# Performance work log

Hardware: AMD Instinct MI355X
Metric: run time of the kernel (lower is better)

Reference implementation:

```python
import jax, jax.numpy as jnp
import numpy as np


def _gtconv(A, w):
    # A: [E,N,N], w: [C,E,1,1]; torch: sum(A * softmax(w, dim=1), dim=1) -> [C,N,N]
    s = jax.nn.softmax(w[:, :, 0, 0], axis=1)  # [C,E]
    return jnp.einsum('enm,ce->cnm', A, s)


def _norm_row(H):
    # row-normalize (H + I): D^-1 (H + I)
    n = H.shape[0]
    H = H + jnp.eye(n, dtype=H.dtype)
    deg = jnp.sum(H, axis=1)
    deg = jnp.where(deg <= 1e-10, 1.0, deg)
    return H / deg[:, None]


def _sgc(feature, adj):
    # D^-1/2 (adj + 2I) D^-1/2 @ feature  (diag scaling, same math as torch's dense mm with diag)
    n = adj.shape[0]
    adj = adj + 2.0 * jnp.eye(n, dtype=adj.dtype)
    deg = jnp.sum(adj, axis=1)
    deg = jnp.where(deg <= 1e-10, 1.0, deg)
    dinv = deg ** -0.5
    adj = adj * dinv[:, None] * dinv[None, :]
    return adj @ feature


def setup_inputs() -> dict:
    key = jax.random.key(0)
    ks = jax.random.split(key, 20)
    E, C, N, D, P, F = 5, 2, 3000, 1000, 2000, 128
    inp = {
        'A': jax.random.uniform(ks[0], (E, N, N), dtype=jnp.float32),
        'DTI': jax.random.uniform(ks[1], (N, N), dtype=jnp.float32),
        'drug_structure': jax.random.normal(ks[2], (D, F), dtype=jnp.float32),
        'protein_structure': jax.random.normal(ks[3], (P, F), dtype=jnp.float32),
        'gt_w0a': jax.random.normal(ks[4], (C, E, 1, 1), dtype=jnp.float32),
        'gt_w0b': jax.random.normal(ks[5], (C, E, 1, 1), dtype=jnp.float32),
        'gt_w1': jax.random.normal(ks[6], (C, E, 1, 1), dtype=jnp.float32),
        'a_param': jnp.ones((C + 1, 1, 1), dtype=jnp.float32),
        'drug_num': D,
        'protein_num': P,
    }
    lin_keys = jax.random.split(ks[7], 12)
    names = ['wd1', 'bd1', 'wd2', 'bd2', 'wd3', 'bd3', 'wp1', 'bp1', 'wp2', 'bp2', 'wp3', 'bp3']
    for i, nm in enumerate(names):
        shp = (F, F) if nm.startswith('w') else (F,)
        inp[nm] = jax.random.normal(lin_keys[i], shp, dtype=jnp.float32) * 0.05
    return inp


def reference(A, DTI, drug_structure, protein_structure, gt_w0a, gt_w0b, gt_w1,
              wd1, bd1, wd2, bd2, wd3, bd3, wp1, bp1, wp2, bp2, wp3, bp3,
              a_param, drug_num, protein_num):
    relu = jax.nn.relu
    drug = relu(drug_structure @ wd1.T + bd1)
    drug = relu(drug @ wd2.T + bd2)
    drug = relu(drug @ wd3.T + bd3)
    prot = relu(protein_structure @ wp1.T + bp1)
    prot = relu(prot @ wp2.T + bp2)
    prot = relu(prot @ wp3.T + bp3)
    feature = jnp.concatenate([drug, prot], axis=0)  # [N,128]

    # GT layers: layer 0 (first=True), layer 1 (first=False)
    a0 = _gtconv(A, gt_w0a)  # [C,N,N]
    b0 = _gtconv(A, gt_w0b)
    H = jnp.matmul(a0, b0)  # bmm
    H = jax.vmap(_norm_row)(H)
    H = jnp.matmul(H, _gtconv(A, gt_w1))

    adj = H  # H[:, :N, :N] is a no-op here
    X_conv1 = _sgc(_sgc(feature, DTI), DTI)
    chs = jax.vmap(lambda a_: _sgc(_sgc(feature, a_), a_))(adj)  # [C,N,128]

    C = adj.shape[0]
    if C == 1:
        X_conv3 = chs
    else:
        order = [0, 1]
        for i in range(2, C):
            order = [i] + order  # torch prepends X_tem for i>=2
        X_conv3 = chs[jnp.array(order)]

    X_conv = jnp.concatenate([X_conv1[None], X_conv3], axis=0)  # [C+1,N,128]
    att = jax.nn.softmax(a_param, axis=0)  # [C+1,1,1]
    conv_sum = jnp.sum(att * X_conv, axis=0)  # [N,128]

    drug_feature = conv_sum[:drug_num]
    protein_feature = conv_sum[drug_num:]
    y = jax.nn.sigmoid(drug_feature @ protein_feature.T)  # [D,P]
    return y
```

## Files before the change

### kernel.cpp

```cpp
#include <hip/hip_runtime.h>
#include <hip/hip_bf16.h>

typedef __attribute__((ext_vector_type(8))) __bf16 bf16x8;
typedef __attribute__((ext_vector_type(4))) float floatx4;

#define NVALID 3000
#define NPAD   3072
#define FEA    128
#define ZSPLIT 8
#define KCHUNK 384
#define PSTRIDE 393216
#define SLOT   ((size_t)ZSPLIT * PSTRIDE)

__device__ __forceinline__ void gload16(const void* g, void* l) {
    __builtin_amdgcn_global_load_lds(
        (const __attribute__((address_space(1))) void*)g,
        (__attribute__((address_space(3))) void*)l,
        16, 0, 0);
}

__device__ __forceinline__ float b2f(__hip_bfloat16 h) { return __bfloat162float(h); }

__global__ __launch_bounds__(256) void mlp_fused(
    const float* __restrict__ Xd, const float* __restrict__ Xp,
    const float* __restrict__ Wd1, const float* __restrict__ bd1,
    const float* __restrict__ Wd2, const float* __restrict__ bd2,
    const float* __restrict__ Wd3, const float* __restrict__ bd3,
    const float* __restrict__ Wp1, const float* __restrict__ bp1,
    const float* __restrict__ Wp2, const float* __restrict__ bp2,
    const float* __restrict__ Wp3, const float* __restrict__ bp3,
    float* __restrict__ Y)
{
    const bool isP = blockIdx.x >= 125;
    const float* X  = isP ? Xp : Xd;
    const float* W1 = isP ? Wp1 : Wd1; const float* b1 = isP ? bp1 : bd1;
    const float* W2 = isP ? Wp2 : Wd2; const float* b2 = isP ? bp2 : bd2;
    const float* W3 = isP ? Wp3 : Wd3; const float* b3 = isP ? bp3 : bd3;
    const int m0loc = (isP ? (blockIdx.x - 125) : blockIdx.x) * 8;
    const int m0out = blockIdx.x * 8;

    __shared__ float S0[8][128], S1[8][128];
    const int t = threadIdx.x;
    for (int s2 = t; s2 < 1024; s2 += 256) {
        int r = s2 >> 7, ii = s2 & 127;
        S0[r][ii] = X[(size_t)(m0loc + r) * 128 + ii];
    }
    __syncthreads();
    const int o = t & 127, rh = t >> 7;

    {
        float a0 = 0.f, a1 = 0.f, a2 = 0.f, a3 = 0.f;
        const float* wr = W1 + (size_t)o * 128;
        for (int i = 0; i < 128; ++i) {
            float w = wr[i];
            a0 += S0[rh + 0][i] * w; a1 += S0[rh + 2][i] * w;
            a2 += S0[rh + 4][i] * w; a3 += S0[rh + 6][i] * w;
        }
        float bo = b1[o];
        S1[rh + 0][o] = fmaxf(a0 + bo, 0.f);
        S1[rh + 2][o] = fmaxf(a1 + bo, 0.f);
        S1[rh + 4][o] = fmaxf(a2 + bo, 0.f);
        S1[rh + 6][o] = fmaxf(a3 + bo, 0.f);
    }
    __syncthreads();
    {
        float a0 = 0.f, a1 = 0.f, a2 = 0.f, a3 = 0.f;
        const float* wr = W2 + (size_t)o * 128;
        for (int i = 0; i < 128; ++i) {
            float w = wr[i];
            a0 += S1[rh + 0][i] * w; a1 += S1[rh + 2][i] * w;
            a2 += S1[rh + 4][i] * w; a3 += S1[rh + 6][i] * w;
        }
        float bo = b2[o];
        S0[rh + 0][o] = fmaxf(a0 + bo, 0.f);
        S0[rh + 2][o] = fmaxf(a1 + bo, 0.f);
        S0[rh + 4][o] = fmaxf(a2 + bo, 0.f);
        S0[rh + 6][o] = fmaxf(a3 + bo, 0.f);
    }
    __syncthreads();
    {
        float a0 = 0.f, a1 = 0.f, a2 = 0.f, a3 = 0.f;
        const float* wr = W3 + (size_t)o * 128;
        for (int i = 0; i < 128; ++i) {
            float w = wr[i];
            a0 += S0[rh + 0][i] * w; a1 += S0[rh + 2][i] * w;
            a2 += S0[rh + 4][i] * w; a3 += S0[rh + 6][i] * w;
        }
        float bo = b3[o];
        Y[(size_t)(m0out + rh + 0) * 128 + o] = fmaxf(a0 + bo, 0.f);
        Y[(size_t)(m0out + rh + 2) * 128 + o] = fmaxf(a1 + bo, 0.f);
        Y[(size_t)(m0out + rh + 4) * 128 + o] = fmaxf(a2 + bo, 0.f);
        Y[(size_t)(m0out + rh + 6) * 128 + o] = fmaxf(a3 + bo, 0.f);
    }
}

__device__ __forceinline__ void softmax5(const float* __restrict__ w, float* s)
{
    float m = w[0];
    #pragma unroll
    for (int e = 1; e < 5; ++e) m = fmaxf(m, w[e]);
    float sum = 0.f;
    #pragma unroll
    for (int e = 0; e < 5; ++e) { s[e] = __expf(w[e] - m); sum += s[e]; }
    float r = 1.f / sum;
    #pragma unroll
    for (int e = 0; e < 5; ++e) s[e] *= r;
}

__global__ __launch_bounds__(384) void gtconv_fused(
    const float* __restrict__ A, const float* __restrict__ w0a,
    const float* __restrict__ w0b, const float* __restrict__ w1,
    __hip_bfloat16* __restrict__ a00, __hip_bfloat16* __restrict__ b00,
    __hip_bfloat16* __restrict__ g10,
    __hip_bfloat16* __restrict__ a01, __hip_bfloat16* __restrict__ b01,
    __hip_bfloat16* __restrict__ g11,
    float* __restrict__ r1v)
{
    float sw[6][5];
    softmax5(w0a + 0, sw[0]); softmax5(w0b + 0, sw[1]); softmax5(w1 + 0, sw[2]);
    softmax5(w0a + 5, sw[3]); softmax5(w0b + 5, sw[4]); softmax5(w1 + 5, sw[5]);

    const int i  = blockIdx.x;
    const int t  = threadIdx.x;
    const int j0 = t * 8;
    float acc[6][8] = {};
    if (i < NVALID && j0 < NVALID) {
        #pragma unroll
        for (int e = 0; e < 5; ++e) {
            const float* Ae = A + (size_t)e * 9000000 + (size_t)i * 3000 + j0;
            float4 v0 = *reinterpret_cast<const float4*>(Ae);
            float4 v1 = *reinterpret_cast<const float4*>(Ae + 4);
            float x[8] = { v0.x, v0.y, v0.z, v0.w, v1.x, v1.y, v1.z, v1.w };
            #pragma unroll
            for (int m = 0; m < 6; ++m) {
                float se = sw[m][e];
                #pragma unroll
                for (int u = 0; u < 8; ++u) acc[m][u] += se * x[u];
            }
        }
    }
    __hip_bfloat16* dsts[6] = { a00, b00, g10, a01, b01, g11 };
    const size_t base = (size_t)i * NPAD + j0;
    float rs[4];
    #pragma unroll
    for (int m = 0; m < 6; ++m) {
        __align__(16) __hip_bfloat16 h[8];
        float s = 0.f;
        #pragma unroll
        for (int u = 0; u < 8; ++u) {
            h[u] = __float2bfloat16(acc[m][u]);
            s += b2f(h[u]);
        }
        *reinterpret_cast<uint4*>(&dsts[m][base]) = *reinterpret_cast<const uint4*>(h);
        if (m == 1) rs[0] = s; else if (m == 2) rs[1] = s;
        else if (m == 4) rs[2] = s; else if (m == 5) rs[3] = s;
    }
    __shared__ float red[6][4];
    #pragma unroll
    for (int q = 0; q < 4; ++q) {
        float s = rs[q];
        #pragma unroll
        for (int off = 32; off > 0; off >>= 1) s += __shfl_down(s, off);
        if ((t & 63) == 0) red[t >> 6][q] = s;
    }
    __syncthreads();
    if (t == 0) {
        #pragma unroll
        for (int q = 0; q < 4; ++q) {
            float s = red[0][q] + red[1][q] + red[2][q]
                    + red[3][q] + red[4][q] + red[5][q];
            r1v[(size_t)q * NPAD + i] = s;
        }
    }
}

__global__ __launch_bounds__(256) void matvec_degA(
    const __hip_bfloat16* __restrict__ a0_0, const __hip_bfloat16* __restrict__ a0_1,
    const __hip_bfloat16* __restrict__ b0_0, const __hip_bfloat16* __restrict__ b0_1,
    const float* __restrict__ r1v,
    float* __restrict__ dinv2, float* __restrict__ mv12)
{
    const int y = blockIdx.y;
    const __hip_bfloat16* M = (y == 0) ? a0_0 : (y == 1) ? a0_1 : (y == 2) ? b0_0 : b0_1;
    const float* v = (y == 0) ? r1v : (y == 1) ? r1v + 2 * NPAD
                   : (y == 2) ? r1v + NPAD : r1v + 3 * NPAD;
    const size_t i = blockIdx.x;
    const int t = threadIdx.x;
    const __hip_bfloat16* row = M + i * NPAD;
    float s = 0.f;
    for (int k = t * 8; k < NPAD; k += 2048) {
        uint4 u = *reinterpret_cast<const uint4*>(&row[k]);
        const unsigned short* us = reinterpret_cast<const unsigned short*>(&u);
        #pragma unroll
        for (int e = 0; e < 8; ++e)
            s += __uint_as_float(((unsigned int)us[e]) << 16) * v[k + e];
    }
    #pragma unroll
    for (int off = 32; off > 0; off >>= 1) s += __shfl_down(s, off);
    __shared__ float red[4];
    if ((t & 63) == 0) red[t >> 6] = s;
    __syncthreads();
    if (t == 0) {
        float tot = red[0] + red[1] + red[2] + red[3];
        if (y < 2) dinv2[(size_t)y * NPAD + i] = 1.f / (tot + 1.f);
        else       mv12[(size_t)(y - 2) * NPAD + i] = tot;
    }
}

__global__ __launch_bounds__(256) void matvec_degB(
    const __hip_bfloat16* __restrict__ a0_0, const __hip_bfloat16* __restrict__ a0_1,
    const float* __restrict__ mv12, const float* __restrict__ dinv2,
    const float* __restrict__ r1v, float* __restrict__ rsv2)
{
    const int c = blockIdx.y;
    const __hip_bfloat16* M = c ? a0_1 : a0_0;
    const float* v = mv12 + (size_t)c * NPAD;
    const float* add = r1v + (size_t)(2 * c + 1) * NPAD;
    const size_t i = blockIdx.x;
    const int t = threadIdx.x;
    const __hip_bfloat16* row = M + i * NPAD;
    float s = 0.f;
    for (int k = t * 8; k < NPAD; k += 2048) {
        uint4 u = *reinterpret_cast<const uint4*>(&row[k]);
        const unsigned short* us = reinterpret_cast<const unsigned short*>(&u);
        #pragma unroll
        for (int e = 0; e < 8; ++e)
            s += __uint_as_float(((unsigned int)us[e]) << 16) * v[k + e];
    }
    #pragma unroll
    for (int off = 32; off > 0; off >>= 1) s += __shfl_down(s, off);
    __shared__ float red[4];
    if ((t & 63) == 0) red[t >> 6] = s;
    __syncthreads();
    if (t == 0) {
        float tot = red[0] + red[1] + red[2] + red[3];
        rsv2[(size_t)c * NPAD + i] =
            rsqrtf(dinv2[(size_t)c * NPAD + i] * (tot + add[i]) + 2.f);
    }
}

__global__ __launch_bounds__(256) void rowdeg_f32(
    const float* __restrict__ src, float* __restrict__ outv)
{
    const int i = blockIdx.x, t = threadIdx.x;
    float s = 0.f;
    if (i < NVALID) {
        const float* row = src + (size_t)i * 3000;
        for (int j4 = t; j4 < 750; j4 += 256) {
            float4 v = *reinterpret_cast<const float4*>(row + j4 * 4);
            s += v.x + v.y + v.z + v.w;
        }
    }
    #pragma unroll
    for (int off = 32; off > 0; off >>= 1) s += __shfl_down(s, off);
    __shared__ float red[4];
    if ((t & 63) == 0) red[t >> 6] = s;
    __syncthreads();
    if (t == 0) {
        float tot = red[0] + red[1] + red[2] + red[3];
        outv[i] = rsqrtf(tot + 2.f);
    }
}

__global__ __launch_bounds__(256) void scale_cast_f32(
    const float* __restrict__ src, int lds_, int nvalid,
    const float* __restrict__ vec, __hip_bfloat16* __restrict__ dst)
{
    const int i = blockIdx.y;
    const int j0 = (blockIdx.x * 256 + threadIdx.x) * 4;
    const float vi = vec[i];
    float v[4];
    if (i < nvalid && j0 + 3 < nvalid) {
        float4 f = *reinterpret_cast<const float4*>(src + (size_t)i * lds_ + j0);
        v[0] = f.x; v[1] = f.y; v[2] = f.z; v[3] = f.w;
    } else {
        #pragma unroll
        for (int u = 0; u < 4; ++u) {
            int j = j0 + u;
            v[u] = (i < nvalid && j < nvalid) ? src[(size_t)i * lds_ + j] : 0.f;
        }
    }
    #pragma unroll
    for (int u = 0; u < 4; ++u) {
        int j = j0 + u;
        if (j == i && i < nvalid) v[u] += 2.f;
        v[u] *= vi * vec[j];
    }
    __align__(8) __hip_bfloat16 h[4];
    #pragma unroll
    for (int u = 0; u < 4; ++u) h[u] = __float2bfloat16(v[u]);
    *reinterpret_cast<uint2*>(&dst[(size_t)i * NPAD + j0]) =
        *reinterpret_cast<const uint2*>(h);
}

__global__ __launch_bounds__(256) void transpose_feat(
    const float* __restrict__ X, int nvalid, __hip_bfloat16* __restrict__ XT)
{
    __shared__ float Ts[32][33];
    const int k0 = blockIdx.x * 32, n0 = blockIdx.y * 32;
    const int t = threadIdx.x, tr = t >> 5, tc = t & 31;
    #pragma unroll
    for (int p = 0; p < 4; ++p) {
        int k = k0 + tr + p * 8;
        Ts[tr + p * 8][tc] = (k < nvalid) ? X[(size_t)k * 128 + n0 + tc] : 0.f;
    }
    __syncthreads();
    #pragma unroll
    for (int p = 0; p < 4; ++p) {
        int n = tr + p * 8;
        XT[(size_t)(n0 + n) * NPAD + k0 + tc] = __float2bfloat16(Ts[tc][n]);
    }
}

__global__ __launch_bounds__(256) void scale_colsT2(
    const __hip_bfloat16* __restrict__ XT, const float* __restrict__ rsv2,
    __hip_bfloat16* __restrict__ W0T_0, __hip_bfloat16* __restrict__ W0T_1)
{
    const int c = blockIdx.z;
    const float* s = rsv2 + (size_t)c * NPAD;
    __hip_bfloat16* W0T = c ? W0T_1 : W0T_0;
    const int f = blockIdx.y;
    const int k0 = (blockIdx.x * 256 + threadIdx.x) * 8;
    if (k0 >= NPAD) return;
    uint4 u = *reinterpret_cast<const uint4*>(&XT[(size_t)f * NPAD + k0]);
    const unsigned short* us = reinterpret_cast<const unsigned short*>(&u);
    __align__(16) __hip_bfloat16 h[8];
    #pragma unroll
    for (int e = 0; e < 8; ++e) {
        float x = __uint_as_float(((unsigned int)us[e]) << 16);
        h[e] = __float2bfloat16(x * s[k0 + e]);
    }
    *reinterpret_cast<uint4*>(&W0T[(size_t)f * NPAD + k0]) =
        *reinterpret_cast<const uint4*>(h);
}

__global__ __launch_bounds__(256, 3) void gemm_pan_batch(
    const __hip_bfloat16* __restrict__ P0, const __hip_bfloat16* __restrict__ M0,
    const __hip_bfloat16* __restrict__ P1, const __hip_bfloat16* __restrict__ M1,
    const __hip_bfloat16* __restrict__ P2, const __hip_bfloat16* __restrict__ M2,
    __hip_bfloat16* __restrict__ part)
{
    const int b  = blockIdx.z / ZSPLIT;
    const int zz = blockIdx.z % ZSPLIT;
    const __hip_bfloat16* P = (b == 0) ? P0 : (b == 1) ? P1 : P2;
    const __hip_bfloat16* M = (b == 0) ? M0 : (b == 1) ? M1 : M2;
    __hip_bfloat16* C = part + (size_t)b * SLOT + (size_t)zz * PSTRIDE;

    __shared__ __align__(16) __hip_bfloat16 As[128 * 32];
    __shared__ __align__(16) __hip_bfloat16 Bs[128 * 32];
    const int t = threadIdx.x;
    const int lane = t & 63;
    const int w = t >> 6;
    const int wm = w >> 1, wn = w & 1;
    const int tn = blockIdx.x;
    const int kbeg = zz * KCHUNK;

    const int srow = lane >> 2;
    const int skg  = (lane & 3) * 8;
    const __hip_bfloat16* Ag = P + (size_t)(w * 32 + srow) * NPAD + skg;
    const __hip_bfloat16* Bg = M + (size_t)(tn * 128 + w * 32 + srow) * NPAD + skg;
    __hip_bfloat16* Al0 = &As[w * 1024];
    __hip_bfloat16* Al1 = &As[w * 1024 + 512];
    __hip_bfloat16* Bl0 = &Bs[w * 1024];
    __hip_bfloat16* Bl1 = &Bs[w * 1024 + 512];

    floatx4 acc[4][4] = {};
// ... 78 lines not shown
        for (int ni = 0; ni < 4; ++ni)
            bfv[ni] = *reinterpret_cast<const bf16x8*>(
                &Bs[(wn * 64 + ni * 16 + (lane & 15)) * 32 + koff]);
        #pragma unroll
        for (int mi = 0; mi < 4; ++mi)
            #pragma unroll
            for (int ni = 0; ni < 4; ++ni)
                acc[mi][ni] = __builtin_amdgcn_mfma_f32_16x16x32_bf16(
                    af[mi], bfv[ni], acc[mi][ni], 0, 0, 0);
    }

    const int r0 = tm * 128 + wm * 64 + ((lane >> 4) << 2);
    const int c0 = tn * 128 + wn * 64 + (lane & 15);
    #pragma unroll
    for (int mi = 0; mi < 4; ++mi)
        #pragma unroll
        for (int ni = 0; ni < 4; ++ni) {
            const int col = c0 + ni * 16;
            #pragma unroll
            for (int r = 0; r < 4; ++r) {
                const int row = r0 + mi * 16 + r;
                if (row < Mvalid && col < Nvalid)
                    C[(size_t)row * ldc + col] =
                        1.f / (1.f + __expf(-acc[mi][ni][r]));
            }
        }
}

__global__ __launch_bounds__(256) void reduce_sum_b(
    const __hip_bfloat16* __restrict__ part,
    __hip_bfloat16* __restrict__ O0, __hip_bfloat16* __restrict__ O1,
    __hip_bfloat16* __restrict__ O2)
{
    const int b = blockIdx.y;
    __hip_bfloat16* O = (b == 0) ? O0 : (b == 1) ? O1 : O2;
    if (!O) return;
    const __hip_bfloat16* Pp = part + (size_t)b * SLOT;
    const size_t idx = ((size_t)blockIdx.x * 256 + threadIdx.x) * 8;
    float s[8] = {};
    #pragma unroll
    for (int z = 0; z < ZSPLIT; ++z) {
        uint4 u = *reinterpret_cast<const uint4*>(&Pp[(size_t)z * PSTRIDE + idx]);
        const unsigned short* us = reinterpret_cast<const unsigned short*>(&u);
        #pragma unroll
        for (int e = 0; e < 8; ++e)
            s[e] += __uint_as_float(((unsigned int)us[e]) << 16);
    }
    __align__(16) __hip_bfloat16 h[8];
    #pragma unroll
    for (int e = 0; e < 8; ++e) h[e] = __float2bfloat16(s[e]);
    *reinterpret_cast<uint4*>(&O[idx]) = *reinterpret_cast<const uint4*>(h);
}

__global__ __launch_bounds__(256) void reduce_att_T(
    const __hip_bfloat16* __restrict__ part, const float* __restrict__ ap,
    float* __restrict__ conv)
{
    __shared__ float Ts[32][33];
    const int i0 = blockIdx.x * 32, f0 = blockIdx.y * 32;
    const int t = threadIdx.x, tr = t >> 5, tc = t & 31;
    float a0 = ap[0], a1 = ap[1], a2 = ap[2];
    float m = fmaxf(a0, fmaxf(a1, a2));
    float e0 = __expf(a0 - m), e1 = __expf(a1 - m), e2 = __expf(a2 - m);
    float att0 = e0 / (e0 + e1 + e2);
    #pragma unroll
    for (int p = 0; p < 4; ++p) {
        int f = f0 + tr + p * 8;
        float s = 0.f;
        #pragma unroll
        for (int z = 0; z < ZSPLIT; ++z)
            s += b2f(part[(size_t)z * PSTRIDE + (size_t)f * NPAD + i0 + tc]);
        Ts[tr + p * 8][tc] = s;
    }
    __syncthreads();
    #pragma unroll
    for (int p = 0; p < 4; ++p) {
        int i = i0 + tr + p * 8;
        conv[(size_t)i * 128 + f0 + tc] = att0 * Ts[tc][tr + p * 8];
    }
}

__global__ __launch_bounds__(256) void combine_mid2(
    const __hip_bfloat16* __restrict__ part,
    const __hip_bfloat16* __restrict__ Z0, const __hip_bfloat16* __restrict__ Z1,
    const __hip_bfloat16* __restrict__ XTF,
    const float* __restrict__ rsv2, const float* __restrict__ dinv2,
    __hip_bfloat16* __restrict__ Wp0, __hip_bfloat16* __restrict__ Wp1)
{
    const int c = blockIdx.y;
    const __hip_bfloat16* Vp = part + (size_t)c * SLOT;
    const __hip_bfloat16* Z  = c ? Z1 : Z0;
    const float* sv = rsv2 + (size_t)c * NPAD;
    const float* dv = dinv2 + (size_t)c * NPAD;
    __hip_bfloat16* Wp = c ? Wp1 : Wp0;

    const size_t idx = ((size_t)blockIdx.x * 256 + threadIdx.x) * 8;
    const int i = (int)(idx % NPAD);
    float s[8] = {};
    #pragma unroll
    for (int z = 0; z < ZSPLIT; ++z) {
        uint4 u = *reinterpret_cast<const uint4*>(&Vp[(size_t)z * PSTRIDE + idx]);
        const unsigned short* us = reinterpret_cast<const unsigned short*>(&u);
        #pragma unroll
        for (int e = 0; e < 8; ++e)
            s[e] += __uint_as_float(((unsigned int)us[e]) << 16);
    }
    uint4 uz = *reinterpret_cast<const uint4*>(&Z[idx]);
    uint4 ux = *reinterpret_cast<const uint4*>(&XTF[idx]);
    const unsigned short* usz = reinterpret_cast<const unsigned short*>(&uz);
    const unsigned short* usx = reinterpret_cast<const unsigned short*>(&ux);
    __align__(16) __hip_bfloat16 h[8];
    #pragma unroll
    for (int e = 0; e < 8; ++e) {
        float vsum = s[e] + __uint_as_float(((unsigned int)usz[e]) << 16);
        float x    = __uint_as_float(((unsigned int)usx[e]) << 16);
        float si = sv[i + e], di = dv[i + e];
        float out1 = si * di * vsum + 2.f * si * si * x;
        h[e] = __float2bfloat16(si * out1);
    }
    *reinterpret_cast<uint4*>(&Wp[idx]) = *reinterpret_cast<const uint4*>(h);
}

__global__ __launch_bounds__(256) void combine_att2_T(
    const __hip_bfloat16* __restrict__ part,
    const __hip_bfloat16* __restrict__ Z2_0, const __hip_bfloat16* __restrict__ Z2_1,
    const __hip_bfloat16* __restrict__ Wp0, const __hip_bfloat16* __restrict__ Wp1,
    const float* __restrict__ rsv2, const float* __restrict__ dinv2,
    const float* __restrict__ ap, float* __restrict__ conv)
{
    __shared__ float Ts[32][33];
    const int i0 = blockIdx.x * 32, f0 = blockIdx.y * 32;
    const int t = threadIdx.x, tr = t >> 5, tc = t & 31;
    float a0 = ap[0], a1 = ap[1], a2 = ap[2];
    float m = fmaxf(a0, fmaxf(a1, a2));
    float e0 = __expf(a0 - m), e1 = __expf(a1 - m), e2 = __expf(a2 - m);
    float inv = 1.f / (e0 + e1 + e2);
    float att1 = e1 * inv, att2 = e2 * inv;
    const int i = i0 + tc;
    float s0i = rsv2[i],        d0i = dinv2[i];
    float s1i = rsv2[NPAD + i], d1i = dinv2[NPAD + i];
    #pragma unroll
    for (int p = 0; p < 4; ++p) {
        int f = f0 + tr + p * 8;
        size_t fi = (size_t)f * NPAD + i;
        float v0 = b2f(Z2_0[fi]);
        float v1 = b2f(Z2_1[fi]);
        #pragma unroll
        for (int z = 0; z < ZSPLIT; ++z) {
            v0 += b2f(part[(size_t)z * PSTRIDE + fi]);
            v1 += b2f(part[SLOT + (size_t)z * PSTRIDE + fi]);
        }
        float o0 = s0i * d0i * v0 + 2.f * s0i * b2f(Wp0[fi]);
        float o1 = s1i * d1i * v1 + 2.f * s1i * b2f(Wp1[fi]);
        Ts[tr + p * 8][tc] = att1 * o0 + att2 * o1;
    }
    __syncthreads();
    #pragma unroll
    for (int p = 0; p < 4; ++p) {
        int i2 = i0 + tr + p * 8;
        conv[(size_t)i2 * 128 + f0 + tc] += Ts[tc][tr + p * 8];
    }
}

__global__ __launch_bounds__(256) void cast_split(
    const float* __restrict__ acc, __hip_bfloat16* __restrict__ dF,
    __hip_bfloat16* __restrict__ pF)
{
    const int idx = blockIdx.x * 256 + threadIdx.x;
    if (idx < 1024 * 128) {
        int r = idx >> 7;
        dF[idx] = __float2bfloat16(r < 1000 ? acc[idx] : 0.f);
    } else {
        int j = idx - 1024 * 128;
        int r = j >> 7;
        pF[j] = __float2bfloat16(r < 2000 ? acc[(size_t)(1000 + r) * 128 + (j & 127)] : 0.f);
    }
}

extern "C" void kernel_launch(void* const* d_in, const int* in_sizes, int n_in,
                              void* d_out, int out_size, void* d_ws, size_t ws_size,
                              hipStream_t stream)
{
    const float* A     = (const float*)d_in[0];
    const float* DTI   = (const float*)d_in[1];
    const float* drugS = (const float*)d_in[2];
    const float* protS = (const float*)d_in[3];
    const float* w0a   = (const float*)d_in[4];
    const float* w0b   = (const float*)d_in[5];
    const float* w1g   = (const float*)d_in[6];
    const float* ap    = (const float*)d_in[7];
    const float* wd1 = (const float*)d_in[10]; const float* bd1 = (const float*)d_in[11];
    const float* wd2 = (const float*)d_in[12]; const float* bd2 = (const float*)d_in[13];
    const float* wd3 = (const float*)d_in[14]; const float* bd3 = (const float*)d_in[15];
    const float* wp1 = (const float*)d_in[16]; const float* bp1 = (const float*)d_in[17];
    const float* wp2 = (const float*)d_in[18]; const float* bp2 = (const float*)d_in[19];
    const float* wp3 = (const float*)d_in[20]; const float* bp3 = (const float*)d_in[21];
    float* out = (float*)d_out;

    const size_t SQ_BF  = (size_t)NPAD * NPAD * 2;
    const size_t PAN_BF = (size_t)128 * NPAD * 2;
    char* p = (char*)d_ws;
    auto alloc = [&](size_t sz) { char* r = p; p += (sz + 255) & ~(size_t)255; return r; };
    __hip_bfloat16* sdti = (__hip_bfloat16*)alloc(SQ_BF);
    __hip_bfloat16* a0c[2], *b0c[2], *g1c[2];
    for (int c = 0; c < 2; ++c) {
        a0c[c] = (__hip_bfloat16*)alloc(SQ_BF);
        b0c[c] = (__hip_bfloat16*)alloc(SQ_BF);
        g1c[c] = (__hip_bfloat16*)alloc(SQ_BF);
    }
    __hip_bfloat16* part = (__hip_bfloat16*)alloc((size_t)3 * SLOT * 2);
    float* r1v   = (float*)alloc((size_t)4 * NPAD * 4);
    float* dinv2 = (float*)alloc((size_t)2 * NPAD * 4);
    float* mv12  = (float*)alloc((size_t)2 * NPAD * 4);
    float* rsv2  = (float*)alloc((size_t)2 * NPAD * 4);
    float* degv  = (float*)alloc((size_t)NPAD * 4);
    float* fb    = (float*)alloc((size_t)NPAD * 128 * 4);
    float* conv  = (float*)alloc((size_t)NPAD * 128 * 4);
    __hip_bfloat16* XTF  = (__hip_bfloat16*)alloc(PAN_BF);
    __hip_bfloat16* XT2  = (__hip_bfloat16*)alloc(PAN_BF);
    __hip_bfloat16* W0T_0 = (__hip_bfloat16*)alloc(PAN_BF);
    __hip_bfloat16* W0T_1 = (__hip_bfloat16*)alloc(PAN_BF);
    __hip_bfloat16* Z_0  = (__hip_bfloat16*)alloc(PAN_BF);
    __hip_bfloat16* Z_1  = (__hip_bfloat16*)alloc(PAN_BF);
    __hip_bfloat16* U_0  = (__hip_bfloat16*)alloc(PAN_BF);
    __hip_bfloat16* U_1  = (__hip_bfloat16*)alloc(PAN_BF);
    __hip_bfloat16* Wp_0 = (__hip_bfloat16*)alloc(PAN_BF);
    __hip_bfloat16* Wp_1 = (__hip_bfloat16*)alloc(PAN_BF);
    __hip_bfloat16* dF = (__hip_bfloat16*)alloc((size_t)1024 * 128 * 2);
    __hip_bfloat16* pF = (__hip_bfloat16*)alloc((size_t)2048 * 128 * 2);
    if ((size_t)(p - (char*)d_ws) > ws_size) return;

    mlp_fused<<<375, 256, 0, stream>>>(drugS, protS,
        wd1, bd1, wd2, bd2, wd3, bd3, wp1, bp1, wp2, bp2, wp3, bp3, fb);
    transpose_feat<<<dim3(96, 4), 256, 0, stream>>>(fb, 3000, XTF);

    gtconv_fused<<<NPAD, 384, 0, stream>>>(A, w0a, w0b, w1g,
        a0c[0], b0c[0], g1c[0], a0c[1], b0c[1], g1c[1], r1v);

    rowdeg_f32<<<NPAD, 256, 0, stream>>>(DTI, degv);
    scale_cast_f32<<<dim3(3, NPAD), 256, 0, stream>>>(DTI, 3000, 3000, degv, sdti);

    matvec_degA<<<dim3(NPAD, 4), 256, 0, stream>>>(a0c[0], a0c[1], b0c[0], b0c[1],
        r1v, dinv2, mv12);
    matvec_degB<<<dim3(NPAD, 2), 256, 0, stream>>>(a0c[0], a0c[1], mv12, dinv2, r1v, rsv2);
    scale_colsT2<<<dim3(2, 128, 2), 256, 0, stream>>>(XTF, rsv2, W0T_0, W0T_1);

    gemm_pan_batch<<<dim3(24, 1, 3 * ZSPLIT), 256, 0, stream>>>(
        XTF, sdti, W0T_0, g1c[0], W0T_1, g1c[1], part);
    reduce_sum_b<<<dim3(192, 3), 256, 0, stream>>>(part, XT2, Z_0, Z_1);

    gemm_pan_batch<<<dim3(24, 1, 3 * ZSPLIT), 256, 0, stream>>>(
        XT2, sdti, Z_0, b0c[0], Z_1, b0c[1], part);
    reduce_att_T<<<dim3(96, 4), 256, 0, stream>>>(part, ap, conv);
    reduce_sum_b<<<dim3(192, 2), 256, 0, stream>>>(part + SLOT, U_0, U_1, nullptr);

    gemm_pan_batch<<<dim3(24, 1, 2 * ZSPLIT), 256, 0, stream>>>(
        U_0, a0c[0], U_1, a0c[1], nullptr, nullptr, part);
    combine_mid2<<<dim3(192, 2), 256, 0, stream>>>(part, Z_0, Z_1, XTF,
        rsv2, dinv2, Wp_0, Wp_1);

    gemm_pan_batch<<<dim3(24, 1, 2 * ZSPLIT), 256, 0, stream>>>(
        Wp_0, g1c[0], Wp_1, g1c[1], nullptr, nullptr, part);
    reduce_sum_b<<<dim3(192, 2), 256, 0, stream>>>(part, Z_0, Z_1, nullptr);
    gemm_pan_batch<<<dim3(24, 1, 2 * ZSPLIT), 256, 0, stream>>>(
        Z_0, b0c[0], Z_1, b0c[1], nullptr, nullptr, part);
    reduce_sum_b<<<dim3(192, 2), 256, 0, stream>>>(part, U_0, U_1, nullptr);
    gemm_pan_batch<<<dim3(24, 1, 2 * ZSPLIT), 256, 0, stream>>>(
        U_0, a0c[0], U_1, a0c[1], nullptr, nullptr, part);
    combine_att2_T<<<dim3(96, 4), 256, 0, stream>>>(part, Z_0, Z_1, Wp_0, Wp_1,
        rsv2, dinv2, ap, conv);

    cast_split<<<1536, 256, 0, stream>>>(conv, dF, pF);
    gemm_sig<<<dim3(16, 8), 256, 0, stream>>>(dF, pF, out, 128, 128, 128, 2000, 1000, 2000);
}
```

Baseline: 267.4 us.

## Merge independent small kernels into horizontally fused launches to cut launch count

Independent kernels are merged into combined launches that branch on block index. The gtconv, DTI row-degree and MLP work become one kernel, and the feature transpose, DTI scale-cast and degree matvec become another. The two reductions after the second GEMM are merged, and the final attention combine now writes the bf16 split outputs directly, removing cast_split. The aim is to cut kernel launch and tail overhead and one round trip of conv through memory, at the cost of heterogeneous blocks sharing one launch configuration, with the MLP branch leaving 128 of its 384 threads idle.

```diff
diff --git a/kernel.cpp b/kernel.cpp
--- a/kernel.cpp
+++ b/kernel.cpp
@@ -21,7 +21,28 @@
 
 __device__ __forceinline__ float b2f(__hip_bfloat16 h) { return __bfloat162float(h); }
 
-__global__ __launch_bounds__(256) void mlp_fused(
+__device__ __forceinline__ void softmax5(const float* __restrict__ w, float* s)
+{
+    float m = w[0];
+    #pragma unroll
+    for (int e = 1; e < 5; ++e) m = fmaxf(m, w[e]);
+    float sum = 0.f;
+    #pragma unroll
+    for (int e = 0; e < 5; ++e) { s[e] = __expf(w[e] - m); sum += s[e]; }
+    float r = 1.f / sum;
+    #pragma unroll
+    for (int e = 0; e < 5; ++e) s[e] *= r;
+}
+
+__global__ __launch_bounds__(384) void head_fused(
+    const float* __restrict__ A, const float* __restrict__ w0a,
+    const float* __restrict__ w0b, const float* __restrict__ w1,
+    __hip_bfloat16* __restrict__ a00, __hip_bfloat16* __restrict__ b00,
+    __hip_bfloat16* __restrict__ g10,
+    __hip_bfloat16* __restrict__ a01, __hip_bfloat16* __restrict__ b01,
+    __hip_bfloat16* __restrict__ g11,
+    float* __restrict__ r1v,
+    const float* __restrict__ DTI, float* __restrict__ degv,
     const float* __restrict__ Xd, const float* __restrict__ Xp,
     const float* __restrict__ Wd1, const float* __restrict__ bd1,
     const float* __restrict__ Wd2, const float* __restrict__ bd2,
@@ -31,179 +52,229 @@
     const float* __restrict__ Wp3, const float* __restrict__ bp3,
     float* __restrict__ Y)
 {
-    const bool isP = blockIdx.x >= 125;
-    const float* X  = isP ? Xp : Xd;
-    const float* W1 = isP ? Wp1 : Wd1; const float* b1 = isP ? bp1 : bd1;
-    const float* W2 = isP ? Wp2 : Wd2; const float* b2 = isP ? bp2 : bd2;
-    const float* W3 = isP ? Wp3 : Wd3; const float* b3 = isP ? bp3 : bd3;
-    const int m0loc = (isP ? (blockIdx.x - 125) : blockIdx.x) * 8;
-    const int m0out = blockIdx.x * 8;
-
-    __shared__ float S0[8][128], S1[8][128];
+    const int bid = blockIdx.x;
     const int t = threadIdx.x;
-    for (int s2 = t; s2 < 1024; s2 += 256) {
-        int r = s2 >> 7, ii = s2 & 127;
-        S0[r][ii] = X[(size_t)(m0loc + r) * 128 + ii];
-    }
-    __syncthreads();
-    const int o = t & 127, rh = t >> 7;
-
-    {
-        float a0 = 0.f, a1 = 0.f, a2 = 0.f, a3 = 0.f;
-        const float* wr = W1 + (size_t)o * 128;
-        for (int i = 0; i < 128; ++i) {
-            float w = wr[i];
-            a0 += S0[rh + 0][i] * w; a1 += S0[rh + 2][i] * w;
-            a2 += S0[rh + 4][i] * w; a3 += S0[rh + 6][i] * w;
-        }
-        float bo = b1[o];
-        S1[rh + 0][o] = fmaxf(a0 + bo, 0.f);
-        S1[rh + 2][o] = fmaxf(a1 + bo, 0.f);
-        S1[rh + 4][o] = fmaxf(a2 + bo, 0.f);
-        S1[rh + 6][o] = fmaxf(a3 + bo, 0.f);
-    }
-    __syncthreads();
-    {
-        float a0 = 0.f, a1 = 0.f, a2 = 0.f, a3 = 0.f;
-        const float* wr = W2 + (size_t)o * 128;
-        for (int i = 0; i < 128; ++i) {
-            float w = wr[i];
-            a0 += S1[rh + 0][i] * w; a1 += S1[rh + 2][i] * w;
-            a2 += S1[rh + 4][i] * w; a3 += S1[rh + 6][i] * w;
-        }
-        float bo = b2[o];
-        S0[rh + 0][o] = fmaxf(a0 + bo, 0.f);
-        S0[rh + 2][o] = fmaxf(a1 + bo, 0.f);
-        S0[rh + 4][o] = fmaxf(a2 + bo, 0.f);
-        S0[rh + 6][o] = fmaxf(a3 + bo, 0.f);
-    }
-    __syncthreads();
-    {
-        float a0 = 0.f, a1 = 0.f, a2 = 0.f, a3 = 0.f;
-        const float* wr = W3 + (size_t)o * 128;
-        for (int i = 0; i < 128; ++i) {
-            float w = wr[i];
-            a0 += S0[rh + 0][i] * w; a1 += S0[rh + 2][i] * w;
-            a2 += S0[rh + 4][i] * w; a3 += S0[rh + 6][i] * w;
-        }
-        float bo = b3[o];
-        Y[(size_t)(m0out + rh + 0) * 128 + o] = fmaxf(a0 + bo, 0.f);
-        Y[(size_t)(m0out + rh + 2) * 128 + o] = fmaxf(a1 + bo, 0.f);
-        Y[(size_t)(m0out + rh + 4) * 128 + o] = fmaxf(a2 + bo, 0.f);
-        Y[(size_t)(m0out + rh + 6) * 128 + o] = fmaxf(a3 + bo, 0.f);
-    }
-}
-
-__device__ __forceinline__ void softmax5(const float* __restrict__ w, float* s)
-{
-    float m = w[0];
-    #pragma unroll
-    for (int e = 1; e < 5; ++e) m = fmaxf(m, w[e]);
-    float sum = 0.f;
-    #pragma unroll
-    for (int e = 0; e < 5; ++e) { s[e] = __expf(w[e] - m); sum += s[e]; }
-    float r = 1.f / sum;
-    #pragma unroll
-    for (int e = 0; e < 5; ++e) s[e] *= r;
-}
-
-__global__ __launch_bounds__(384) void gtconv_fused(
-    const float* __restrict__ A, const float* __restrict__ w0a,
-    const float* __restrict__ w0b, const float* __restrict__ w1,
-    __hip_bfloat16* __restrict__ a00, __hip_bfloat16* __restrict__ b00,
-    __hip_bfloat16* __restrict__ g10,
-    __hip_bfloat16* __restrict__ a01, __hip_bfloat16* __restrict__ b01,
-    __hip_bfloat16* __restrict__ g11,
-    float* __restrict__ r1v)
-{
-    float sw[6][5];
-    softmax5(w0a + 0, sw[0]); softmax5(w0b + 0, sw[1]); softmax5(w1 + 0, sw[2]);
-    softmax5(w0a + 5, sw[3]); softmax5(w0b + 5, sw[4]); softmax5(w1 + 5, sw[5]);
-
-    const int i  = blockIdx.x;
-    const int t  = threadIdx.x;
-    const int j0 = t * 8;
-    float acc[6][8] = {};
-    if (i < NVALID && j0 < NVALID) {
-        #pragma unroll
-        for (int e = 0; e < 5; ++e) {
-            const float* Ae = A + (size_t)e * 9000000 + (size_t)i * 3000 + j0;
-            float4 v0 = *reinterpret_cast<const float4*>(Ae);
-            float4 v1 = *reinterpret_cast<const float4*>(Ae + 4);
-            float x[8] = { v0.x, v0.y, v0.z, v0.w, v1.x, v1.y, v1.z, v1.w };
-            #pragma unroll
-            for (int m = 0; m < 6; ++m) {
-                float se = sw[m][e];
+
+    if (bid < NPAD) {
+        float sw[6][5];
+        softmax5(w0a + 0, sw[0]); softmax5(w0b + 0, sw[1]); softmax5(w1 + 0, sw[2]);
+        softmax5(w0a + 5, sw[3]); softmax5(w0b + 5, sw[4]); softmax5(w1 + 5, sw[5]);
+
+        const int i  = bid;
+        const int j0 = t * 8;
+        float acc[6][8] = {};
+        if (i < NVALID && j0 < NVALID) {
+            #pragma unroll
+            for (int e = 0; e < 5; ++e) {
+                const float* Ae = A + (size_t)e * 9000000 + (size_t)i * 3000 + j0;
+                float4 v0 = *reinterpret_cast<const float4*>(Ae);
+                float4 v1 = *reinterpret_cast<const float4*>(Ae + 4);
+                float x[8] = { v0.x, v0.y, v0.z, v0.w, v1.x, v1.y, v1.z, v1.w };
                 #pragma unroll
-                for (int u = 0; u < 8; ++u) acc[m][u] += se * x[u];
-            }
-        }
-    }
-    __hip_bfloat16* dsts[6] = { a00, b00, g10, a01, b01, g11 };
-    const size_t base = (size_t)i * NPAD + j0;
-    float rs[4];
-    #pragma unroll
-    for (int m = 0; m < 6; ++m) {
-        __align__(16) __hip_bfloat16 h[8];
+                for (int m = 0; m < 6; ++m) {
+                    float se = sw[m][e];
+                    #pragma unroll
+                    for (int u = 0; u < 8; ++u) acc[m][u] += se * x[u];
+                }
+            }
+        }
+        __hip_bfloat16* dsts[6] = { a00, b00, g10, a01, b01, g11 };
+        const size_t base = (size_t)i * NPAD + j0;
+        float rs[4];
+        #pragma unroll
+        for (int m = 0; m < 6; ++m) {
+            __align__(16) __hip_bfloat16 h[8];
+            float s = 0.f;
+            #pragma unroll
+            for (int u = 0; u < 8; ++u) {
+                h[u] = __float2bfloat16(acc[m][u]);
+                s += b2f(h[u]);
+            }
+            *reinterpret_cast<uint4*>(&dsts[m][base]) = *reinterpret_cast<const uint4*>(h);
+            if (m == 1) rs[0] = s; else if (m == 2) rs[1] = s;
+            else if (m == 4) rs[2] = s; else if (m == 5) rs[3] = s;
+        }
+        __shared__ float redg[6][4];
+        #pragma unroll
+        for (int q = 0; q < 4; ++q) {
+            float s = rs[q];
+            #pragma unroll
+            for (int off = 32; off > 0; off >>= 1) s += __shfl_down(s, off);
+            if ((t & 63) == 0) redg[t >> 6][q] = s;
+        }
+        __syncthreads();
+        if (t == 0) {
+            #pragma unroll
+            for (int q = 0; q < 4; ++q) {
+                float s = redg[0][q] + redg[1][q] + redg[2][q]
+                        + redg[3][q] + redg[4][q] + redg[5][q];
+                r1v[(size_t)q * NPAD + i] = s;
+            }
+        }
+    } else if (bid < 2 * NPAD) {
+        const int i = bid - NPAD;
         float s = 0.f;
-        #pragma unroll
-        for (int u = 0; u < 8; ++u) {
-            h[u] = __float2bfloat16(acc[m][u]);
-            s += b2f(h[u]);
-        }
-        *reinterpret_cast<uint4*>(&dsts[m][base]) = *reinterpret_cast<const uint4*>(h);
-        if (m == 1) rs[0] = s; else if (m == 2) rs[1] = s;
-        else if (m == 4) rs[2] = s; else if (m == 5) rs[3] = s;
-    }
-    __shared__ float red[6][4];
-    #pragma unroll
-    for (int q = 0; q < 4; ++q) {
-        float s = rs[q];
+        if (i < NVALID) {
+            const float* row = DTI + (size_t)i * 3000;
+            for (int j4 = t; j4 < 750; j4 += 384) {
+                float4 v = *reinterpret_cast<const float4*>(row + j4 * 4);
+                s += v.x + v.y + v.z + v.w;
+            }
+        }
         #pragma unroll
         for (int off = 32; off > 0; off >>= 1) s += __shfl_down(s, off);
-        if ((t & 63) == 0) red[t >> 6][q] = s;
-    }
-    __syncthreads();
-    if (t == 0) {
-        #pragma unroll
-        for (int q = 0; q < 4; ++q) {
-            float s = red[0][q] + red[1][q] + red[2][q]
-                    + red[3][q] + red[4][q] + red[5][q];
-            r1v[(size_t)q * NPAD + i] = s;
-        }
-    }
-}
-
-__global__ __launch_bounds__(256) void matvec_degA(
+        __shared__ float redd[6];
+        if ((t & 63) == 0) redd[t >> 6] = s;
+        __syncthreads();
+        if (t == 0) {
+            float tot = redd[0] + redd[1] + redd[2] + redd[3] + redd[4] + redd[5];
+            degv[i] = rsqrtf(tot + 2.f);
+        }
+    } else {
+        const int blk = bid - 2 * NPAD;
+        const bool isP = blk >= 125;
+        const float* X  = isP ? Xp : Xd;
+        const float* W1 = isP ? Wp1 : Wd1; const float* b1 = isP ? bp1 : bd1;
+        const float* W2 = isP ? Wp2 : Wd2; const float* b2 = isP ? bp2 : bd2;
+        const float* W3 = isP ? Wp3 : Wd3; const float* b3 = isP ? bp3 : bd3;
+        const int m0loc = (isP ? (blk - 125) : blk) * 8;
+        const int m0out = blk * 8;
+
+        __shared__ float S0[8][128], S1m[8][128];
+        for (int s2 = t; s2 < 1024; s2 += 384) {
+            int r = s2 >> 7, ii = s2 & 127;
+            S0[r][ii] = X[(size_t)(m0loc + r) * 128 + ii];
+        }
+        __syncthreads();
+        const int o = t & 127, rh = t >> 7;
+        if (t < 256) {
+            float a0 = 0.f, a1 = 0.f, a2 = 0.f, a3 = 0.f;
+            const float* wr = W1 + (size_t)o * 128;
+            for (int i = 0; i < 128; ++i) {
+                float w = wr[i];
+                a0 += S0[rh + 0][i] * w; a1 += S0[rh + 2][i] * w;
+                a2 += S0[rh + 4][i] * w; a3 += S0[rh + 6][i] * w;
+            }
+            float bo = b1[o];
+            S1m[rh + 0][o] = fmaxf(a0 + bo, 0.f);
+            S1m[rh + 2][o] = fmaxf(a1 + bo, 0.f);
+            S1m[rh + 4][o] = fmaxf(a2 + bo, 0.f);
+            S1m[rh + 6][o] = fmaxf(a3 + bo, 0.f);
+        }
+        __syncthreads();
+        if (t < 256) {
+            float a0 = 0.f, a1 = 0.f, a2 = 0.f, a3 = 0.f;
+            const float* wr = W2 + (size_t)o * 128;
+            for (int i = 0; i < 128; ++i) {
+                float w = wr[i];
+                a0 += S1m[rh + 0][i] * w; a1 += S1m[rh + 2][i] * w;
+                a2 += S1m[rh + 4][i] * w; a3 += S1m[rh + 6][i] * w;
+            }
+            float bo = b2[o];
+            S0[rh + 0][o] = fmaxf(a0 + bo, 0.f);
+            S0[rh + 2][o] = fmaxf(a1 + bo, 0.f);
+            S0[rh + 4][o] = fmaxf(a2 + bo, 0.f);
+            S0[rh + 6][o] = fmaxf(a3 + bo, 0.f);
+        }
+        __syncthreads();
+        if (t < 256) {
+            float a0 = 0.f, a1 = 0.f, a2 = 0.f, a3 = 0.f;
+            const float* wr = W3 + (size_t)o * 128;
+            for (int i = 0; i < 128; ++i) {
+                float w = wr[i];
+                a0 += S0[rh + 0][i] * w; a1 += S0[rh + 2][i] * w;
+                a2 += S0[rh + 4][i] * w; a3 += S0[rh + 6][i] * w;
+            }
+            float bo = b3[o];
+            Y[(size_t)(m0out + rh + 0) * 128 + o] = fmaxf(a0 + bo, 0.f);
+            Y[(size_t)(m0out + rh + 2) * 128 + o] = fmaxf(a1 + bo, 0.f);
+            Y[(size_t)(m0out + rh + 4) * 128 + o] = fmaxf(a2 + bo, 0.f);
+            Y[(size_t)(m0out + rh + 6) * 128 + o] = fmaxf(a3 + bo, 0.f);
+        }
+    }
+}
+
+__global__ __launch_bounds__(256) void mid_fused(
+    const float* __restrict__ fb, __hip_bfloat16* __restrict__ XTF,
+    const float* __restrict__ DTI, const float* __restrict__ degv,
+    __hip_bfloat16* __restrict__ sdti,
     const __hip_bfloat16* __restrict__ a0_0, const __hip_bfloat16* __restrict__ a0_1,
     const __hip_bfloat16* __restrict__ b0_0, const __hip_bfloat16* __restrict__ b0_1,
     const float* __restrict__ r1v,
     float* __restrict__ dinv2, float* __restrict__ mv12)
 {
-    const int y = blockIdx.y;
-    const __hip_bfloat16* M = (y == 0) ? a0_0 : (y == 1) ? a0_1 : (y == 2) ? b0_0 : b0_1;
-    const float* v = (y == 0) ? r1v : (y == 1) ? r1v + 2 * NPAD
-                   : (y == 2) ? r1v + NPAD : r1v + 3 * NPAD;
-    const size_t i = blockIdx.x;
+    const int bid = blockIdx.x;
     const int t = threadIdx.x;
-    const __hip_bfloat16* row = M + i * NPAD;
-    float s = 0.f;
-    for (int k = t * 8; k < NPAD; k += 2048) {
-        uint4 u = *reinterpret_cast<const uint4*>(&row[k]);
-        const unsigned short* us = reinterpret_cast<const unsigned short*>(&u);
-        #pragma unroll
-        for (int e = 0; e < 8; ++e)
-            s += __uint_as_float(((unsigned int)us[e]) << 16) * v[k + e];
-    }
-    #pragma unroll
-    for (int off = 32; off > 0; off >>= 1) s += __shfl_down(s, off);
-    __shared__ float red[4];
-    if ((t & 63) == 0) red[t >> 6] = s;
-    __syncthreads();
-    if (t == 0) {
-        float tot = red[0] + red[1] + red[2] + red[3];
-        if (y < 2) dinv2[(size_t)y * NPAD + i] = 1.f / (tot + 1.f);
-        else       mv12[(size_t)(y - 2) * NPAD + i] = tot;
+
+    if (bid < 384) {
+        __shared__ float Ts[32][33];
+        const int k0 = (bid % 96) * 32, n0 = (bid / 96) * 32;
+        const int tr = t >> 5, tc = t & 31;
+        #pragma unroll
+        for (int p = 0; p < 4; ++p) {
+            int k = k0 + tr + p * 8;
+            Ts[tr + p * 8][tc] = (k < NVALID) ? fb[(size_t)k * 128 + n0 + tc] : 0.f;
+        }
+        __syncthreads();
+        #pragma unroll
+        for (int p = 0; p < 4; ++p) {
+            int n = tr + p * 8;
+            XTF[(size_t)(n0 + n) * NPAD + k0 + tc] = __float2bfloat16(Ts[tc][n]);
+        }
+    } else if (bid < 9600) {
+        const int r = bid - 384;
+        const int i = r / 3;
+        const int j0 = ((r % 3) * 256 + t) * 4;
+        const float vi = degv[i];
+        float v[4];
+        if (i < NVALID && j0 + 3 < NVALID) {
+            float4 f = *reinterpret_cast<const float4*>(DTI + (size_t)i * 3000 + j0);
+            v[0] = f.x; v[1] = f.y; v[2] = f.z; v[3] = f.w;
+        } else {
+            #pragma unroll
+            for (int u = 0; u < 4; ++u) {
+                int j = j0 + u;
+                v[u] = (i < NVALID && j < NVALID) ? DTI[(size_t)i * 3000 + j] : 0.f;
+            }
+        }
+        #pragma unroll
+        for (int u = 0; u < 4; ++u) {
+            int j = j0 + u;
+            if (j == i && i < NVALID) v[u] += 2.f;
+            v[u] *= vi * degv[j];
+        }
+        __align__(8) __hip_bfloat16 h[4];
+        #pragma unroll
+        for (int u = 0; u < 4; ++u) h[u] = __float2bfloat16(v[u]);
+        *reinterpret_cast<uint2*>(&sdti[(size_t)i * NPAD + j0]) =
+            *reinterpret_cast<const uint2*>(h);
+    } else {
+        const int r = bid - 9600;
+        const int y = r / NPAD;
+        const size_t i = r % NPAD;
+        const __hip_bfloat16* M = (y == 0) ? a0_0 : (y == 1) ? a0_1
+                                : (y == 2) ? b0_0 : b0_1;
+        const float* v = (y == 0) ? r1v : (y == 1) ? r1v + 2 * NPAD
+                       : (y == 2) ? r1v + NPAD : r1v + 3 * NPAD;
+        const __hip_bfloat16* row = M + i * NPAD;
+        float s = 0.f;
+        for (int k = t * 8; k < NPAD; k += 2048) {
+            uint4 u = *reinterpret_cast<const uint4*>(&row[k]);
+            const unsigned short* us = reinterpret_cast<const unsigned short*>(&u);
+            #pragma unroll
+            for (int e = 0; e < 8; ++e)
+                s += __uint_as_float(((unsigned int)us[e]) << 16) * v[k + e];
+        }
+        #pragma unroll
+        for (int off = 32; off > 0; off >>= 1) s += __shfl_down(s, off);
+        __shared__ float red[4];
+        if ((t & 63) == 0) red[t >> 6] = s;
+        __syncthreads();
+        if (t == 0) {
+            float tot = red[0] + red[1] + red[2] + red[3];
+            if (y < 2) dinv2[(size_t)y * NPAD + i] = 1.f / (tot + 1.f);
+            else       mv12[(size_t)(y - 2) * NPAD + i] = tot;
+        }
     }
 }
 
@@ -239,79 +310,6 @@
     }
 }
 
-__global__ __launch_bounds__(256) void rowdeg_f32(
-    const float* __restrict__ src, float* __restrict__ outv)
-{
-    const int i = blockIdx.x, t = threadIdx.x;
-    float s = 0.f;
-    if (i < NVALID) {
-        const float* row = src + (size_t)i * 3000;
-        for (int j4 = t; j4 < 750; j4 += 256) {
-            float4 v = *reinterpret_cast<const float4*>(row + j4 * 4);
-            s += v.x + v.y + v.z + v.w;
-        }
-    }
-    #pragma unroll
-    for (int off = 32; off > 0; off >>= 1) s += __shfl_down(s, off);
-    __shared__ float red[4];
-    if ((t & 63) == 0) red[t >> 6] = s;
-    __syncthreads();
-    if (t == 0) {
-        float tot = red[0] + red[1] + red[2] + red[3];
-        outv[i] = rsqrtf(tot + 2.f);
-    }
-}
-
-__global__ __launch_bounds__(256) void scale_cast_f32(
-    const float* __restrict__ src, int lds_, int nvalid,
-    const float* __restrict__ vec, __hip_bfloat16* __restrict__ dst)
-{
-    const int i = blockIdx.y;
-    const int j0 = (blockIdx.x * 256 + threadIdx.x) * 4;
-    const float vi = vec[i];
-    float v[4];
-    if (i < nvalid && j0 + 3 < nvalid) {
-        float4 f = *reinterpret_cast<const float4*>(src + (size_t)i * lds_ + j0);
-        v[0] = f.x; v[1] = f.y; v[2] = f.z; v[3] = f.w;
-    } else {
-        #pragma unroll
-        for (int u = 0; u < 4; ++u) {
-            int j = j0 + u;
-            v[u] = (i < nvalid && j < nvalid) ? src[(size_t)i * lds_ + j] : 0.f;
-        }
-    }
-    #pragma unroll
-    for (int u = 0; u < 4; ++u) {
-        int j = j0 + u;
-        if (j == i && i < nvalid) v[u] += 2.f;
-        v[u] *= vi * vec[j];
-    }
-    __align__(8) __hip_bfloat16 h[4];
-    #pragma unroll
-    for (int u = 0; u < 4; ++u) h[u] = __float2bfloat16(v[u]);
-    *reinterpret_cast<uint2*>(&dst[(size_t)i * NPAD + j0]) =
-        *reinterpret_cast<const uint2*>(h);
-}
-
-__global__ __launch_bounds__(256) void transpose_feat(
-    const float* __restrict__ X, int nvalid, __hip_bfloat16* __restrict__ XT)
-{
-    __shared__ float Ts[32][33];
-    const int k0 = blockIdx.x * 32, n0 = blockIdx.y * 32;
-    const int t = threadIdx.x, tr = t >> 5, tc = t & 31;
-    #pragma unroll
-    for (int p = 0; p < 4; ++p) {
-        int k = k0 + tr + p * 8;
-        Ts[tr + p * 8][tc] = (k < nvalid) ? X[(size_t)k * 128 + n0 + tc] : 0.f;
-    }
-    __syncthreads();
-    #pragma unroll
-    for (int p = 0; p < 4; ++p) {
-        int n = tr + p * 8;
-        XT[(size_t)(n0 + n) * NPAD + k0 + tc] = __float2bfloat16(Ts[tc][n]);
-    }
-}
-
 __global__ __launch_bounds__(256) void scale_colsT2(
     const __hip_bfloat16* __restrict__ XT, const float* __restrict__ rsv2,
     __hip_bfloat16* __restrict__ W0T_0, __hip_bfloat16* __restrict__ W0T_1)
@@ -496,31 +494,55 @@
     *reinterpret_cast<uint4*>(&O[idx]) = *reinterpret_cast<const uint4*>(h);
 }
 
-__global__ __launch_bounds__(256) void reduce_att_T(
+__global__ __launch_bounds__(256) void reduce_s2(
     const __hip_bfloat16* __restrict__ part, const float* __restrict__ ap,
-    float* __restrict__ conv)
-{
-    __shared__ float Ts[32][33];
-    const int i0 = blockIdx.x * 32, f0 = blockIdx.y * 32;
-    const int t = threadIdx.x, tr = t >> 5, tc = t & 31;
-    float a0 = ap[0], a1 = ap[1], a2 = ap[2];
-    float m = fmaxf(a0, fmaxf(a1, a2));
-    float e0 = __expf(a0 - m), e1 = __expf(a1 - m), e2 = __expf(a2 - m);
-    float att0 = e0 / (e0 + e1 + e2);
-    #pragma unroll
-    for (int p = 0; p < 4; ++p) {
-        int f = f0 + tr + p * 8;
-        float s = 0.f;
-        #pragma unroll
-        for (int z = 0; z < ZSPLIT; ++z)
-            s += b2f(part[(size_t)z * PSTRIDE + (size_t)f * NPAD + i0 + tc]);
-        Ts[tr + p * 8][tc] = s;
-    }
-    __syncthreads();
-    #pragma unroll
-    for (int p = 0; p < 4; ++p) {
-        int i = i0 + tr + p * 8;
-        conv[(size_t)i * 128 + f0 + tc] = att0 * Ts[tc][tr + p * 8];
+    float* __restrict__ conv,
+    __hip_bfloat16* __restrict__ U0, __hip_bfloat16* __restrict__ U1)
+{
+    const int bid = blockIdx.x;
+    const int t = threadIdx.x;
+    if (bid < 384) {
+        __shared__ float Ts[32][33];
+        const int i0 = (bid % 96) * 32, f0 = (bid / 96) * 32;
+        const int tr = t >> 5, tc = t & 31;
+        float a0 = ap[0], a1 = ap[1], a2 = ap[2];
+        float m = fmaxf(a0, fmaxf(a1, a2));
+        float e0 = __expf(a0 - m), e1 = __expf(a1 - m), e2 = __expf(a2 - m);
+        float att0 = e0 / (e0 + e1 + e2);
+        #pragma unroll
+        for (int p = 0; p < 4; ++p) {
+            int f = f0 + tr + p * 8;
+            float s = 0.f;
+            #pragma unroll
+            for (int z = 0; z < ZSPLIT; ++z)
+                s += b2f(part[(size_t)z * PSTRIDE + (size_t)f * NPAD + i0 + tc]);
+            Ts[tr + p * 8][tc] = s;
+        }
+        __syncthreads();
+        #pragma unroll
+        for (int p = 0; p < 4; ++p) {
+            int i = i0 + tr + p * 8;
+            conv[(size_t)i * 128 + f0 + tc] = att0 * Ts[tc][tr + p * 8];
+        }
+    } else {
+        const int r = bid - 384;
+        const int b = r / 192;
+        __hip_bfloat16* O = b ? U1 : U0;
+        const __hip_bfloat16* Pp = part + (size_t)(b + 1) * SLOT;
+        const size_t idx = ((size_t)(r % 192) * 256 + t) * 8;
+        float s[8] = {};
+        #pragma unroll
+        for (int z = 0; z < ZSPLIT; ++z) {
+            uint4 u = *reinterpret_cast<const uint4*>(&Pp[(size_t)z * PSTRIDE + idx]);
+            const unsigned short* us = reinterpret_cast<const unsigned short*>(&u);
+            #pragma unroll
+            for (int e = 0; e < 8; ++e)
+                s[e] += __uint_as_float(((unsigned int)us[e]) << 16);
+        }
+        __align__(16) __hip_bfloat16 h[8];
+        #pragma unroll
+        for (int e = 0; e < 8; ++e) h[e] = __float2bfloat16(s[e]);
+        *reinterpret_cast<uint4*>(&O[idx]) = *reinterpret_cast<const uint4*>(h);
     }
 }
 
@@ -565,12 +587,13 @@
     *reinterpret_cast<uint4*>(&Wp[idx]) = *reinterpret_cast<const uint4*>(h);
 }
 
-__global__ __launch_bounds__(256) void combine_att2_T(
+__global__ __launch_bounds__(256) void combine_att2_cast(
     const __hip_bfloat16* __restrict__ part,
     const __hip_bfloat16* __restrict__ Z2_0, const __hip_bfloat16* __restrict__ Z2_1,
     const __hip_bfloat16* __restrict__ Wp0, const __hip_bfloat16* __restrict__ Wp1,
     const float* __restrict__ rsv2, const float* __restrict__ dinv2,
-    const float* __restrict__ ap, float* __restrict__ conv)
+    const float* __restrict__ ap, const float* __restrict__ conv,
+    __hip_bfloat16* __restrict__ dF, __hip_bfloat16* __restrict__ pF)
 {
     __shared__ float Ts[32][33];
     const int i0 = blockIdx.x * 32, f0 = blockIdx.y * 32;
@@ -602,22 +625,17 @@
     #pragma unroll
     for (int p = 0; p < 4; ++p) {
         int i2 = i0 + tr + p * 8;
-        conv[(size_t)i2 * 128 + f0 + tc] += Ts[tc][tr + p * 8];
-    }
-}
-
-__global__ __launch_bounds__(256) void cast_split(
-    const float* __restrict__ acc, __hip_bfloat16* __restrict__ dF,
-    __hip_bfloat16* __restrict__ pF)
-{
-    const int idx = blockIdx.x * 256 + threadIdx.x;
-    if (idx < 1024 * 128) {
-        int r = idx >> 7;
-        dF[idx] = __float2bfloat16(r < 1000 ? acc[idx] : 0.f);
-    } else {
-        int j = idx - 1024 * 128;
-        int r = j >> 7;
-        pF[j] = __float2bfloat16(r < 2000 ? acc[(size_t)(1000 + r) * 128 + (j & 127)] : 0.f);
+        int f = f0 + tc;
+        float v = conv[(size_t)i2 * 128 + f] + Ts[tc][tr + p * 8];
+        if (i2 < 1000) {
+            dF[(size_t)i2 * 128 + f] = __float2bfloat16(v);
+        } else {
+            if (i2 < 1024) dF[(size_t)i2 * 128 + f] = __float2bfloat16(0.f);
+            int pr = i2 - 1000;
+            if (pr < 2048)
+                pF[(size_t)pr * 128 + f] =
+                    __float2bfloat16(i2 < NVALID ? v : 0.f);
+        }
     }
 }
 
@@ -674,18 +692,17 @@
     __hip_bfloat16* pF = (__hip_bfloat16*)alloc((size_t)2048 * 128 * 2);
     if ((size_t)(p - (char*)d_ws) > ws_size) return;
 
-    mlp_fused<<<375, 256, 0, stream>>>(drugS, protS,
-        wd1, bd1, wd2, bd2, wd3, bd3, wp1, bp1, wp2, bp2, wp3, bp3, fb);
-    transpose_feat<<<dim3(96, 4), 256, 0, stream>>>(fb, 3000, XTF);
-
-    gtconv_fused<<<NPAD, 384, 0, stream>>>(A, w0a, w0b, w1g,
-        a0c[0], b0c[0], g1c[0], a0c[1], b0c[1], g1c[1], r1v);
-
-    rowdeg_f32<<<NPAD, 256, 0, stream>>>(DTI, degv);
-    scale_cast_f32<<<dim3(3, NPAD), 256, 0, stream>>>(DTI, 3000, 3000, degv, sdti);
-
-    matvec_degA<<<dim3(NPAD, 4), 256, 0, stream>>>(a0c[0], a0c[1], b0c[0], b0c[1],
-        r1v, dinv2, mv12);
+    head_fused<<<2 * NPAD + 375, 384, 0, stream>>>(
+        A, w0a, w0b, w1g,
+        a0c[0], b0c[0], g1c[0], a0c[1], b0c[1], g1c[1], r1v,
+        DTI, degv,
+        drugS, protS, wd1, bd1, wd2, bd2, wd3, bd3,
+        wp1, bp1, wp2, bp2, wp3, bp3, fb);
+
+    mid_fused<<<21888, 256, 0, stream>>>(
+        fb, XTF, DTI, degv, sdti,
+        a0c[0], a0c[1], b0c[0], b0c[1], r1v, dinv2, mv12);
+
     matvec_degB<<<dim3(NPAD, 2), 256, 0, stream>>>(a0c[0], a0c[1], mv12, dinv2, r1v, rsv2);
     scale_colsT2<<<dim3(2, 128, 2), 256, 0, stream>>>(XTF, rsv2, W0T_0, W0T_1);
 
@@ -695,8 +712,7 @@
 
     gemm_pan_batch<<<dim3(24, 1, 3 * ZSPLIT), 256, 0, stream>>>(
         XT2, sdti, Z_0, b0c[0], Z_1, b0c[1], part);
-    reduce_att_T<<<dim3(96, 4), 256, 0, stream>>>(part, ap, conv);
-    reduce_sum_b<<<dim3(192, 2), 256, 0, stream>>>(part + SLOT, U_0, U_1, nullptr);
+    reduce_s2<<<768, 256, 0, stream>>>(part, ap, conv, U_0, U_1);
 
     gemm_pan_batch<<<dim3(24, 1, 2 * ZSPLIT), 256, 0, stream>>>(
         U_0, a0c[0], U_1, a0c[1], nullptr, nullptr, part);
@@ -711,9 +727,8 @@
     reduce_sum_b<<<dim3(192, 2), 256, 0, stream>>>(part, U_0, U_1, nullptr);
     gemm_pan_batch<<<dim3(24, 1, 2 * ZSPLIT), 256, 0, stream>>>(
         U_0, a0c[0], U_1, a0c[1], nullptr, nullptr, part);
-    combine_att2_T<<<dim3(96, 4), 256, 0, stream>>>(part, Z_0, Z_1, Wp_0, Wp_1,
-        rsv2, dinv2, ap, conv);
-
-    cast_split<<<1536, 256, 0, stream>>>(conv, dF, pF);
+    combine_att2_cast<<<dim3(96, 4), 256, 0, stream>>>(part, Z_0, Z_1, Wp_0, Wp_1,
+        rsv2, dinv2, ap, conv, dF, pF);
+
     gemm_sig<<<dim3(16, 8), 256, 0, stream>>>(dF, pF, out, 128, 128, 128, 2000, 1000, 2000);
 }
```

Measured after the change: 257.6 us (median of 2 runs). 3.7% less time.
